# Kernel tuning notes

Measured on AMD Instinct MI355X. Metric: run time of the kernel, lower is better.

Reference implementation:

```python
import jax, jax.numpy as jnp
import numpy as np

B, S, D_MODEL, H = 2, 2048, 1024, 16
D_K = D_MODEL // H
THETA = 10000.0


def setup_inputs() -> dict:
    key = jax.random.key(0)
    k1, k2, k3 = jax.random.split(key, 3)
    x = jax.random.normal(k1, (B, S, D_MODEL), dtype=jnp.float32)
    token_positions = jnp.tile(jnp.arange(S, dtype=jnp.int32), (B, 1))
    qkv_w = jax.random.normal(k2, (3 * D_MODEL, D_MODEL), dtype=jnp.float32) * (D_MODEL ** -0.5)
    out_w = jax.random.normal(k3, (D_MODEL, D_MODEL), dtype=jnp.float32) * (D_MODEL ** -0.5)
    return {"x": x, "token_positions": token_positions, "qkv_w": qkv_w, "out_w": out_w}


def _apply_rope(t, pos):
    # t: [B, H, S, d_k], pos: [B, S]
    half = D_K // 2
    inv_freq = THETA ** (-jnp.arange(0, half, dtype=jnp.float32) * 2.0 / D_K)  # [half]
    ang = pos.astype(jnp.float32)[:, None, :, None] * inv_freq  # [B,1,S,half]
    cos, sin = jnp.cos(ang), jnp.sin(ang)
    t1 = t[..., 0::2]
    t2 = t[..., 1::2]
    r1 = t1 * cos - t2 * sin
    r2 = t1 * sin + t2 * cos
    # interleave back: [..., half, 2] -> [..., d_k]
    return jnp.stack([r1, r2], axis=-1).reshape(t.shape)


def reference(x, token_positions, qkv_w, out_w):
    # fused QKV projection (no bias)
    qkv = jnp.einsum('bsd,ed->bse', x, qkv_w)  # [B,S,3*D_MODEL]
    qkv = qkv.reshape(B, S, 3, H, D_K)
    q = jnp.transpose(qkv[:, :, 0], (0, 2, 1, 3))  # [B,H,S,d_k]
    k = jnp.transpose(qkv[:, :, 1], (0, 2, 1, 3))
    v = jnp.transpose(qkv[:, :, 2], (0, 2, 1, 3))
    q = _apply_rope(q, token_positions)
    k = _apply_rope(k, token_positions)
    scores = jnp.einsum('bhqd,bhkd->bhqk', q, k) / jnp.sqrt(jnp.asarray(D_K, x.dtype))
    causal = jnp.tril(jnp.ones((S, S), dtype=bool))
    neg_inf = jnp.finfo(scores.dtype).min
    scores = jnp.where(causal, scores, neg_inf)
    attn = jax.nn.softmax(scores, axis=-1)
    out = jnp.einsum('bhqk,bhkd->bhqd', attn, v)  # [B,H,S,d_k]
    out = jnp.transpose(out, (0, 2, 1, 3)).reshape(B, S, D_MODEL)
    return jnp.einsum('bsd,ed->bse', out, out_w)
```

## Files before the change

### kernel.cpp

```cpp
#include <hip/hip_runtime.h>
#include <cstdint>

typedef unsigned short u16;
typedef unsigned int u32;
typedef __attribute__((ext_vector_type(8))) short short8;
typedef __attribute__((ext_vector_type(4))) float f32x4;

static constexpr int Bc = 2, Sc = 2048, DMc = 1024, Hc = 16, DKc = 64;
static constexpr int Mc = Bc * Sc;
static constexpr int BHSc = Bc * Hc * Sc;

#if __has_builtin(__builtin_amdgcn_exp2f)
#define EXP2F(x) __builtin_amdgcn_exp2f(x)
#else
#define EXP2F(x) exp2f(x)
#endif

__device__ __forceinline__ float b2f(u16 u) { return __uint_as_float((u32)u << 16); }
__device__ __forceinline__ u16 f2b(float f) {
  u32 x = __float_as_uint(f);
  return (u16)((x + 0x7fffu + ((x >> 16) & 1u)) >> 16);
}
__device__ __forceinline__ u32 pack2(float lo, float hi) {
  return (u32)f2b(lo) | ((u32)f2b(hi) << 16);
}
__device__ __forceinline__ u32 cvtpk(float lo, float hi) {
  u32 r;
  asm("v_cvt_pk_bf16_f32 %0, %1, %2" : "=v"(r) : "v"(lo), "v"(hi));
  return r;
}

__global__ __launch_bounds__(256)
void cvt3_k(const float* __restrict__ x, const float* __restrict__ qw,
            const float* __restrict__ ow,
            u16* __restrict__ xb, u16* __restrict__ qwb, u16* __restrict__ owb)
{
  const int i = blockIdx.x * 256 + threadIdx.x;
  const float* src; u16* dst; int j;
  if (i < 524288)      { src = x;  dst = xb;  j = i; }
  else if (i < 917504) { src = qw; dst = qwb; j = i - 524288; }
  else                 { src = ow; dst = owb; j = i - 917504; }
  const float4 a = *(const float4*)(src + (size_t)j * 8);
  const float4 b = *(const float4*)(src + (size_t)j * 8 + 4);
  uint4 o;
  o.x = cvtpk(a.x, a.y);
  o.y = cvtpk(a.z, a.w);
  o.z = cvtpk(b.x, b.y);
  o.w = cvtpk(b.z, b.w);
  *(uint4*)(dst + (size_t)j * 8) = o;
}

template <typename OutT>
__global__ __launch_bounds__(256, 2)
void gemm_bt128(const u16* __restrict__ A, const u16* __restrict__ W,
                OutT* __restrict__ C, int M, int N, int K)
{
  __shared__ u16 As[128 * 32];
  __shared__ u16 Bs[128 * 32];
  const int t = threadIdx.x;
  const int w = t >> 6, l = t & 63;
  const int wr = w >> 1, wc = w & 1;
  const int l4 = l >> 4, l15 = l & 15;
  const int bm = blockIdx.x, bn = blockIdx.y;

  f32x4 acc[4][4] = {};

  const int rowA = bm * 128, rowB = bn * 128;
  const int sr = l >> 2, sk = (l & 3) * 8;

  for (int k0 = 0; k0 < K; k0 += 32) {
    __syncthreads();
#pragma unroll
    for (int i = 0; i < 2; ++i) {
      const int chunk = i * 4 + w;
      const u16* ga = A + (size_t)(rowA + chunk * 16 + sr) * K + k0 + sk;
      const u16* gb = W + (size_t)(rowB + chunk * 16 + sr) * K + k0 + sk;
      __builtin_amdgcn_global_load_lds((const __attribute__((address_space(1))) void*)ga,
                                       (__attribute__((address_space(3))) void*)(As + chunk * 512), 16, 0, 0);
      __builtin_amdgcn_global_load_lds((const __attribute__((address_space(1))) void*)gb,
                                       (__attribute__((address_space(3))) void*)(Bs + chunk * 512), 16, 0, 0);
    }
    __syncthreads();
    short8 af[4], bf[4];
#pragma unroll
    for (int m = 0; m < 4; ++m)
      af[m] = *(const short8*)(As + (wr * 64 + m * 16 + l15) * 32 + l4 * 8);
#pragma unroll
    for (int n = 0; n < 4; ++n)
      bf[n] = *(const short8*)(Bs + (wc * 64 + n * 16 + l15) * 32 + l4 * 8);
#pragma unroll
    for (int m = 0; m < 4; ++m)
#pragma unroll
      for (int n = 0; n < 4; ++n)
        acc[m][n] = __builtin_amdgcn_mfma_f32_16x16x32_bf16(af[m], bf[n], acc[m][n], 0, 0, 0);
  }

#pragma unroll
  for (int m = 0; m < 4; ++m) {
    const int r0 = rowA + wr * 64 + m * 16 + l4 * 4;
#pragma unroll
    for (int n = 0; n < 4; ++n) {
      const int c0 = rowB + wc * 64 + n * 16 + l15;
#pragma unroll
      for (int r = 0; r < 4; ++r) {
        const float v = acc[m][n][r];
        if constexpr (sizeof(OutT) == 2)
          C[(size_t)(r0 + r) * N + c0] = (OutT)f2b(v);
        else
          C[(size_t)(r0 + r) * N + c0] = (OutT)v;
      }
    }
  }
}

__global__ void rope_table_k(float2* __restrict__ tab)
{
  const int idx = blockIdx.x * 256 + threadIdx.x;
  const int p = idx >> 5, i = idx & 31;
  const float invf = powf(10000.0f, -(float)(2 * i) / 64.0f);
  const float ang = (float)p * invf;
  tab[idx] = make_float2(cosf(ang), sinf(ang));
}

__global__ __launch_bounds__(256)
void rope_reshape_k(const u16* __restrict__ qkv, const int* __restrict__ tokpos,
                    const float2* __restrict__ tab,
                    u16* __restrict__ Q, u16* __restrict__ K, u16* __restrict__ Vt)
{
  __shared__ u16 Vs[64][72];
  const int t = threadIdx.x;
  const int st = blockIdx.x, h = blockIdx.y, b = blockIdx.z;

  {
    const int sl = t >> 2, iq = t & 3;
    const int s = st * 64 + sl;
    const int p = tokpos[b * Sc + s];
    const size_t row = (size_t)(b * Sc + s) * 3 * DMc + h * DKc + iq * 16;
    const size_t orow = ((size_t)(b * Hc + h) * Sc + s) * DKc + iq * 16;
#pragma unroll
    for (int which = 0; which < 2; ++which) {
      const u16* g = qkv + row + which * DMc;
      uint4 va = *(const uint4*)g;
      uint4 vb = *(const uint4*)(g + 8);
      u32 in[8] = {va.x, va.y, va.z, va.w, vb.x, vb.y, vb.z, vb.w};
      const float scale = (which == 0) ? 0.18033688011112f : 1.0f;
      u32 ow[8];
#pragma unroll
      for (int j = 0; j < 8; ++j) {
        const float2 cs = tab[p * 32 + iq * 8 + j];
        const float t1 = b2f((u16)(in[j] & 0xffffu));
        const float t2 = b2f((u16)(in[j] >> 16));
        ow[j] = cvtpk((t1 * cs.x - t2 * cs.y) * scale, (t1 * cs.y + t2 * cs.x) * scale);
      }
      u16* dst = (which == 0 ? Q : K) + orow;
      *(uint4*)dst = make_uint4(ow[0], ow[1], ow[2], ow[3]);
      *(uint4*)(dst + 8) = make_uint4(ow[4], ow[5], ow[6], ow[7]);
    }
  }
#pragma unroll
  for (int it = 0; it < 2; ++it) {
    const int sv = it * 32 + (t >> 3);
    const int d0 = (t & 7) * 8;
    const u16* g = qkv + (size_t)(b * Sc + st * 64 + sv) * 3 * DMc + 2 * DMc + h * DKc + d0;
    *(uint4*)&Vs[sv][d0] = *(const uint4*)g;
  }
  __syncthreads();
  {
    const int d = t >> 2, s0 = (t & 3) * 16;
    u16 tmp[16];
#pragma unroll
    for (int j = 0; j < 16; ++j) tmp[j] = Vs[s0 + j][d];
    u16* dst = Vt + ((size_t)(b * Hc + h) * DKc + d) * Sc + st * 64 + s0;
    *(uint4*)dst = *(const uint4*)tmp;
    *(uint4*)(dst + 8) = *(const uint4*)(tmp + 8);
  }
}

__global__ __launch_bounds__(256, 4)
void attn_k(const u16* __restrict__ Q, const u16* __restrict__ K,
            const u16* __restrict__ Vt, float* __restrict__ Opart,
            float2* __restrict__ ML)
{
  __shared__ u16 Kls[2][64 * 64];
  __shared__ u16 Vls[2][64 * 64];

  const int t = threadIdx.x, w = t >> 6, l = t & 63;
  const int l4 = l >> 4, l15 = l & 15;

  int bid = blockIdx.x;
  bid = (bid & 7) * 128 + (bid >> 3);
  const int p = bid & 15, part = (bid >> 4) & 1, h = (bid >> 5) & 15, b = bid >> 9;

  const int bh = b * Hc + h;
  const u16* Qb = Q + (size_t)bh * Sc * DKc;
  const u16* Kb = K + (size_t)bh * Sc * DKc;
  const u16* Vb = Vt + (size_t)bh * DKc * Sc;
  const int swz = (l15 & 7) << 4;

  const int qt0 = 31 - p, qt1 = p;
  const int q00 = qt0 * 64 + w * 16, q01 = qt1 * 64 + w * 16;
  const int n0 = (qt0 + 2 - part) >> 1, n1 = (qt1 + 2 - part) >> 1;
  const int ntot = n0 + n1;

  const short8 qf0a = *(const short8*)(Qb + (size_t)(q00 + l15) * DKc + l4 * 8);
  const short8 qf0b = *(const short8*)(Qb + (size_t)(q00 + l15) * DKc + 32 + l4 * 8);
  const short8 qf1a = *(const short8*)(Qb + (size_t)(q01 + l15) * DKc + l4 * 8);
  const short8 qf1b = *(const short8*)(Qb + (size_t)(q01 + l15) * DKc + 32 + l4 * 8);

  int srow[2], scol[2];
#pragma unroll
  for (int j = 0; j < 2; ++j) {
    const int e = j * 256 + t;
    srow[j] = e >> 3;
    scol[j] = (((e & 7) * 16) ^ ((srow[j] & 7) << 4)) >> 1;
  }
  auto stage = [&](int buf, int kv0) {
#pragma unroll
    for (int j = 0; j < 2; ++j) {
      const u16* gk = Kb + (size_t)(kv0 + srow[j]) * DKc + scol[j];
      __builtin_amdgcn_global_load_lds((const __attribute__((address_space(1))) void*)gk,
          (__attribute__((address_space(3))) void*)(&Kls[buf][0] + (j * 256 + w * 64) * 8), 16, 0, 0);
    }
#pragma unroll
    for (int j = 0; j < 2; ++j) {
      const u16* gv = Vb + (size_t)srow[j] * Sc + kv0 + scol[j];
      __builtin_amdgcn_global_load_lds((const __attribute__((address_space(1))) void*)gv,
          (__attribute__((address_space(3))) void*)(&Vls[buf][0] + (j * 256 + w * 64) * 8), 16, 0, 0);
    }
  };
  auto kvof = [&](int i) {
    return ((i < n0) ? (part + 2 * i) : (part + 2 * (i - n0))) * 64;
  };

  f32x4 o[4] = {};
  float m = -1e30f, lsum = 0.f;
  int qcur = q00;
  short8 qfA = qf0a, qfB = qf0b;

  auto epi = [&](int qbase) {
    const size_t pbase = ((size_t)part * Bc * Hc + bh) * Sc;
    if (l < 16) ML[pbase + qbase + l15] = make_float2(m, lsum);
#pragma unroll
    for (int dc = 0; dc < 4; ++dc)
#pragma unroll
      for (int r = 0; r < 4; ++r)
        Opart[(pbase + qbase + l4 * 4 + r) * 64 + dc * 16 + l15] = o[dc][r];
  };

  stage(0, kvof(0));
  for (int i = 0; i < ntot; ++i) {
    const int buf = i & 1;
    const int kv0 = kvof(i);
    if (i + 1 < ntot) {
      stage(buf ^ 1, kvof(i + 1));
      asm volatile("s_waitcnt vmcnt(4)" ::: "memory");
    } else {
      asm volatile("s_waitcnt vmcnt(0)" ::: "memory");
    }
    __builtin_amdgcn_s_barrier();

    const char* Kbuf = (const char*)&Kls[buf][0];
    const char* Vbuf = (const char*)&Vls[buf][0];
    char* Pw = (char*)&Kls[buf][0] + w * 2048;

    f32x4 sc[4];
    __builtin_amdgcn_s_setprio(1);
#pragma unroll
    for (int c = 0; c < 4; ++c) {
      const int rb = (c * 16 + l15) * 128;
      const short8 ka  = *(const short8*)(Kbuf + rb + ((l4 * 16) ^ swz));
      const short8 kb2 = *(const short8*)(Kbuf + rb + ((64 + l4 * 16) ^ swz));
      f32x4 z = {0.f, 0.f, 0.f, 0.f};
      z = __builtin_amdgcn_mfma_f32_16x16x32_bf16(ka, qfA, z, 0, 0, 0);
      z = __builtin_amdgcn_mfma_f32_16x16x32_bf16(kb2, qfB, z, 0, 0, 0);
      sc[c] = z;
    }
    __builtin_amdgcn_s_setprio(0);
    if (kv0 + 63 > qcur) {
#pragma unroll
      for (int c = 0; c < 4; ++c) {
        const int kvr = kv0 + c * 16 + l4 * 4;
#pragma unroll
        for (int r = 0; r < 4; ++r)
          if (kvr + r > qcur + l15) sc[c][r] = -1e30f;
      }
    }
    float pmax = -1e30f;
#pragma unroll
    for (int c = 0; c < 4; ++c)
      pmax = fmaxf(pmax, fmaxf(fmaxf(sc[c][0], sc[c][1]), fmaxf(sc[c][2], sc[c][3])));
    pmax = fmaxf(pmax, __shfl_xor(pmax, 16));
    pmax = fmaxf(pmax, __shfl_xor(pmax, 32));
    if (!__all(pmax - m <= 8.0f)) {
      const float mnew = fmaxf(m, pmax);
      const float fac = EXP2F(m - mnew);
      float f4[4];
#pragma unroll
      for (int r = 0; r < 4; ++r) f4[r] = __shfl(fac, l4 * 4 + r);
#pragma unroll
      for (int dc = 0; dc < 4; ++dc) {
        o[dc][0] *= f4[0]; o[dc][1] *= f4[1];
        o[dc][2] *= f4[2]; o[dc][3] *= f4[3];
      }
      lsum *= fac;
      m = mnew;
    }
    float rs = 0.f;
    u32 pk[4][2];
#pragma unroll
    for (int c = 0; c < 4; ++c) {
      const float p0 = EXP2F(sc[c][0] - m);
      const float p1 = EXP2F(sc[c][1] - m);
      const float p2 = EXP2F(sc[c][2] - m);
      const float p3 = EXP2F(sc[c][3] - m);
      rs += (p0 + p1) + (p2 + p3);
      pk[c][0] = cvtpk(p0, p1);
      pk[c][1] = cvtpk(p2, p3);
    }
    rs += __shfl_xor(rs, 16);
    rs += __shfl_xor(rs, 32);
    lsum += rs;

    asm volatile("s_waitcnt lgkmcnt(0)" ::: "memory");
    __builtin_amdgcn_s_barrier();

#pragma unroll
    for (int c = 0; c < 4; ++c) {
      uint2 u; u.x = pk[c][0]; u.y = pk[c][1];
      *(uint2*)(Pw + ((l15 * 128 + c * 32 + l4 * 8) ^ swz)) = u;
    }
    __builtin_amdgcn_s_setprio(1);
#pragma unroll
    for (int kv2 = 0; kv2 < 2; ++kv2) {
      const short8 pa = *(const short8*)(Pw + ((l15 * 128 + kv2 * 64 + l4 * 16) ^ swz));
#pragma unroll
      for (int dc = 0; dc < 4; ++dc) {
        const short8 vf = *(const short8*)(Vbuf + (dc * 16 + l15) * 128 + ((kv2 * 64 + l4 * 16) ^ swz));
        o[dc] = __builtin_amdgcn_mfma_f32_16x16x32_bf16(pa, vf, o[dc], 0, 0, 0);
      }
    }
    __builtin_amdgcn_s_setprio(0);
    asm volatile("s_waitcnt lgkmcnt(0)" ::: "memory");
    __builtin_amdgcn_s_barrier();

    if (i == n0 - 1) {
      epi(q00);
#pragma unroll
      for (int dc = 0; dc < 4; ++dc) o[dc] = f32x4{0.f, 0.f, 0.f, 0.f};
      m = -1e30f; lsum = 0.f;
      qcur = q01; qfA = qf1a; qfB = qf1b;
    }
  }
  epi(q01);
}

__global__ __launch_bounds__(256)
void combine_k(const float* __restrict__ Opart, const float2* __restrict__ ML,
               u16* __restrict__ Oa)
{
  const int idx = blockIdx.x * 256 + threadIdx.x;
  const int row = idx >> 4, c4 = idx & 15;
  const float2 a = ML[row], bm = ML[BHSc + row];
  const float m = fmaxf(a.x, bm.x);
  const float w0 = EXP2F(a.x - m), w1 = EXP2F(bm.x - m);
  const float inv = 1.0f / (w0 * a.y + w1 * bm.y);
  const float4 o0 = *(const float4*)(Opart + (size_t)row * 64 + c4 * 4);
  const float4 o1 = *(const float4*)(Opart + ((size_t)BHSc + row) * 64 + c4 * 4);
  const float r0 = (w0 * o0.x + w1 * o1.x) * inv;
  const float r1 = (w0 * o0.y + w1 * o1.y) * inv;
  const float r2 = (w0 * o0.z + w1 * o1.z) * inv;
  const float r3 = (w0 * o0.w + w1 * o1.w) * inv;
  const int s = row & (Sc - 1), bh = row >> 11, b = bh >> 4, h = bh & 15;
  uint2 pk;
  pk.x = cvtpk(r0, r1);
  pk.y = cvtpk(r2, r3);
  *(uint2*)(Oa + ((size_t)(b * Sc + s) * DMc + h * DKc + c4 * 4)) = pk;
}

extern "C" void kernel_launch(void* const* d_in, const int* in_sizes, int n_in,
                              void* d_out, int out_size, void* d_ws, size_t ws_size,
                              hipStream_t stream)
{
  const float* x      = (const float*)d_in[0];
  const int*   tokpos = (const int*)d_in[1];
  const float* qkv_w  = (const float*)d_in[2];
  const float* out_w  = (const float*)d_in[3];
  float* out = (float*)d_out;

  char* ws = (char*)d_ws;
  size_t off = 0;
  u16*   qkv   = (u16*)(ws + off);
  u16*   xb    = (u16*)(ws + off + 25165824);
  u16*   qwb   = (u16*)(ws + off + 33554432);
  float* Opart = (float*)(ws + off);
  float2* ML   = (float2*)(ws + off + 33554432);
  off += 39845888;
  u16* owb = (u16*)(ws + off); off += (size_t)DMc * DMc * 2;
  u16* Qr  = (u16*)(ws + off); off += (size_t)Bc * Hc * Sc * DKc * 2;
  u16* Kr  = (u16*)(ws + off); off += (size_t)Bc * Hc * Sc * DKc * 2;
  u16* Vt  = (u16*)(ws + off); off += (size_t)Bc * Hc * DKc * Sc * 2;
  u16* Oa  = (u16*)(ws + off); off += (size_t)Mc * DMc * 2;
  float2* tab = (float2*)(ws + off); off += (size_t)Sc * 32 * sizeof(float2);

  cvt3_k<<<4096, 256, 0, stream>>>(x, qkv_w, out_w, xb, qwb, owb);
  rope_table_k<<<(Sc * 32) / 256, 256, 0, stream>>>(tab);
  gemm_bt128<u16><<<dim3(Mc / 128, 3 * DMc / 128), 256, 0, stream>>>(xb, qwb, qkv, Mc, 3 * DMc, DMc);
  rope_reshape_k<<<dim3(Sc / 64, Hc, Bc), 256, 0, stream>>>(qkv, tokpos, tab, Qr, Kr, Vt);
  attn_k<<<1024, 256, 0, stream>>>(Qr, Kr, Vt, Opart, ML);
  combine_k<<<BHSc * 16 / 256, 256, 0, stream>>>(Opart, ML, Oa);
  gemm_bt128<float><<<dim3(Mc / 128, DMc / 128), 256, 0, stream>>>(Oa, owb, out, Mc, DMc, DMc);
}
```

Before: 125.9 us.

## Fuse RoPE and head reshape into QKV GEMM epilogue; store attention partials as bf16

The QKV GEMM epilogue now applies RoPE (using lane shuffles to pair even and odd dims), the Q scale, and the head-major scatter directly. This removes the intermediate qkv buffer and the separate rope/reshape pass. V is still written head-major and transposed by a smaller vtrans kernel. The attention partial outputs are also stored as bf16 instead of fp32, halving combine traffic at some precision cost. The epilogue writes remain scalar 2-byte stores with strided addresses, which may be poorly coalesced.

```diff
diff --git a/kernel.cpp b/kernel.cpp
--- a/kernel.cpp
+++ b/kernel.cpp
@@ -17,13 +17,6 @@
 #endif
 
 __device__ __forceinline__ float b2f(u16 u) { return __uint_as_float((u32)u << 16); }
-__device__ __forceinline__ u16 f2b(float f) {
-  u32 x = __float_as_uint(f);
-  return (u16)((x + 0x7fffu + ((x >> 16) & 1u)) >> 16);
-}
-__device__ __forceinline__ u32 pack2(float lo, float hi) {
-  return (u32)f2b(lo) | ((u32)f2b(hi) << 16);
-}
 __device__ __forceinline__ u32 cvtpk(float lo, float hi) {
   u32 r;
   asm("v_cvt_pk_bf16_f32 %0, %1, %2" : "=v"(r) : "v"(lo), "v"(hi));
@@ -50,10 +43,13 @@
   *(uint4*)(dst + (size_t)j * 8) = o;
 }
 
-template <typename OutT>
+template <int EPI>
 __global__ __launch_bounds__(256, 2)
 void gemm_bt128(const u16* __restrict__ A, const u16* __restrict__ W,
-                OutT* __restrict__ C, int M, int N, int K)
+                float* __restrict__ Cf,
+                const int* __restrict__ tokpos, const float2* __restrict__ tab,
+                u16* __restrict__ Qo, u16* __restrict__ Ko, u16* __restrict__ Vo,
+                int M, int N, int K)
 {
   __shared__ u16 As[128 * 32];
   __shared__ u16 Bs[128 * 32];
@@ -95,19 +91,52 @@
         acc[m][n] = __builtin_amdgcn_mfma_f32_16x16x32_bf16(af[m], bf[n], acc[m][n], 0, 0, 0);
   }
 
-#pragma unroll
-  for (int m = 0; m < 4; ++m) {
-    const int r0 = rowA + wr * 64 + m * 16 + l4 * 4;
-#pragma unroll
-    for (int n = 0; n < 4; ++n) {
-      const int c0 = rowB + wc * 64 + n * 16 + l15;
-#pragma unroll
-      for (int r = 0; r < 4; ++r) {
-        const float v = acc[m][n][r];
-        if constexpr (sizeof(OutT) == 2)
-          C[(size_t)(r0 + r) * N + c0] = (OutT)f2b(v);
-        else
-          C[(size_t)(r0 + r) * N + c0] = (OutT)v;
+  if constexpr (EPI == 2) {
+    const int whichW = bn >> 3;
+    const int hh = (bn & 7) * 2 + wc;
+    u16* dst = (whichW == 0) ? Qo : (whichW == 1 ? Ko : Vo);
+    int pos[4][4];
+    if (whichW < 2) {
+#pragma unroll
+      for (int m = 0; m < 4; ++m)
+#pragma unroll
+        for (int r = 0; r < 4; ++r)
+          pos[m][r] = tokpos[rowA + wr * 64 + m * 16 + l4 * 4 + r];
+    }
+#pragma unroll
+    for (int m = 0; m < 4; ++m) {
+#pragma unroll
+      for (int n = 0; n < 4; ++n) {
+        const int d = n * 16 + l15;
+#pragma unroll
+        for (int r = 0; r < 4; ++r) {
+          const int sg = rowA + wr * 64 + m * 16 + l4 * 4 + r;
+          const int bb = sg >> 11, ss = sg & 2047;
+          const size_t addr = ((size_t)(bb * Hc + hh) * Sc + ss) * DKc + d;
+          const float v = acc[m][n][r];
+          if (whichW == 2) {
+            dst[addr] = (u16)cvtpk(v, v);
+          } else {
+            const float vp = __shfl_xor(v, 1);
+            const float2 cs = tab[pos[m][r] * 32 + (d >> 1)];
+            float res = (l15 & 1) ? (vp * cs.y + v * cs.x)
+                                  : (v * cs.x - vp * cs.y);
+            if (whichW == 0) res *= 0.18033688011112f;
+            dst[addr] = (u16)cvtpk(res, res);
+          }
+        }
+      }
+    }
+  } else {
+#pragma unroll
+    for (int m = 0; m < 4; ++m) {
+      const int r0 = rowA + wr * 64 + m * 16 + l4 * 4;
+#pragma unroll
+      for (int n = 0; n < 4; ++n) {
+        const int c0 = rowB + wc * 64 + n * 16 + l15;
+#pragma unroll
+        for (int r = 0; r < 4; ++r)
+          Cf[(size_t)(r0 + r) * N + c0] = acc[m][n][r];
       }
     }
   }
@@ -123,62 +152,31 @@
 }
 
 __global__ __launch_bounds__(256)
-void rope_reshape_k(const u16* __restrict__ qkv, const int* __restrict__ tokpos,
-                    const float2* __restrict__ tab,
-                    u16* __restrict__ Q, u16* __restrict__ K, u16* __restrict__ Vt)
-{
-  __shared__ u16 Vs[64][72];
+void vtrans_k(const u16* __restrict__ Vc, u16* __restrict__ Vt)
+{
+  __shared__ u16 T[64][72];
   const int t = threadIdx.x;
   const int st = blockIdx.x, h = blockIdx.y, b = blockIdx.z;
-
-  {
-    const int sl = t >> 2, iq = t & 3;
-    const int s = st * 64 + sl;
-    const int p = tokpos[b * Sc + s];
-    const size_t row = (size_t)(b * Sc + s) * 3 * DMc + h * DKc + iq * 16;
-    const size_t orow = ((size_t)(b * Hc + h) * Sc + s) * DKc + iq * 16;
-#pragma unroll
-    for (int which = 0; which < 2; ++which) {
-      const u16* g = qkv + row + which * DMc;
-      uint4 va = *(const uint4*)g;
-      uint4 vb = *(const uint4*)(g + 8);
-      u32 in[8] = {va.x, va.y, va.z, va.w, vb.x, vb.y, vb.z, vb.w};
-      const float scale = (which == 0) ? 0.18033688011112f : 1.0f;
-      u32 ow[8];
-#pragma unroll
-      for (int j = 0; j < 8; ++j) {
-        const float2 cs = tab[p * 32 + iq * 8 + j];
-        const float t1 = b2f((u16)(in[j] & 0xffffu));
-        const float t2 = b2f((u16)(in[j] >> 16));
-        ow[j] = cvtpk((t1 * cs.x - t2 * cs.y) * scale, (t1 * cs.y + t2 * cs.x) * scale);
-      }
-      u16* dst = (which == 0 ? Q : K) + orow;
-      *(uint4*)dst = make_uint4(ow[0], ow[1], ow[2], ow[3]);
-      *(uint4*)(dst + 8) = make_uint4(ow[4], ow[5], ow[6], ow[7]);
-    }
-  }
+  const size_t bh = (size_t)b * Hc + h;
 #pragma unroll
   for (int it = 0; it < 2; ++it) {
     const int sv = it * 32 + (t >> 3);
     const int d0 = (t & 7) * 8;
-    const u16* g = qkv + (size_t)(b * Sc + st * 64 + sv) * 3 * DMc + 2 * DMc + h * DKc + d0;
-    *(uint4*)&Vs[sv][d0] = *(const uint4*)g;
+    *(uint4*)&T[sv][d0] = *(const uint4*)(Vc + (bh * Sc + st * 64 + sv) * DKc + d0);
   }
   __syncthreads();
-  {
-    const int d = t >> 2, s0 = (t & 3) * 16;
-    u16 tmp[16];
-#pragma unroll
-    for (int j = 0; j < 16; ++j) tmp[j] = Vs[s0 + j][d];
-    u16* dst = Vt + ((size_t)(b * Hc + h) * DKc + d) * Sc + st * 64 + s0;
-    *(uint4*)dst = *(const uint4*)tmp;
-    *(uint4*)(dst + 8) = *(const uint4*)(tmp + 8);
-  }
+  const int d = t >> 2, s0 = (t & 3) * 16;
+  u16 tmp[16];
+#pragma unroll
+  for (int j = 0; j < 16; ++j) tmp[j] = T[s0 + j][d];
+  u16* dst = Vt + (bh * DKc + d) * Sc + st * 64 + s0;
+  *(uint4*)dst = *(const uint4*)tmp;
+  *(uint4*)(dst + 8) = *(const uint4*)(tmp + 8);
 }
 
 __global__ __launch_bounds__(256, 4)
 void attn_k(const u16* __restrict__ Q, const u16* __restrict__ K,
-            const u16* __restrict__ Vt, float* __restrict__ Opart,
+            const u16* __restrict__ Vt, u16* __restrict__ Opart,
             float2* __restrict__ ML)
 {
   __shared__ u16 Kls[2][64 * 64];
@@ -244,7 +242,8 @@
     for (int dc = 0; dc < 4; ++dc)
 #pragma unroll
       for (int r = 0; r < 4; ++r)
-        Opart[(pbase + qbase + l4 * 4 + r) * 64 + dc * 16 + l15] = o[dc][r];
+        Opart[(pbase + qbase + l4 * 4 + r) * 64 + dc * 16 + l15] =
+            (u16)cvtpk(o[dc][r], o[dc][r]);
   };
 
   stage(0, kvof(0));
@@ -355,21 +354,21 @@
 }
 
 __global__ __launch_bounds__(256)
-void combine_k(const float* __restrict__ Opart, const float2* __restrict__ ML,
+void combine_k(const u16* __restrict__ Opart, const float2* __restrict__ ML,
                u16* __restrict__ Oa)
 {
   const int idx = blockIdx.x * 256 + threadIdx.x;
   const int row = idx >> 4, c4 = idx & 15;
-  const float2 a = ML[row], bm = ML[BHSc + row];
-  const float m = fmaxf(a.x, bm.x);
-  const float w0 = EXP2F(a.x - m), w1 = EXP2F(bm.x - m);
-  const float inv = 1.0f / (w0 * a.y + w1 * bm.y);
-  const float4 o0 = *(const float4*)(Opart + (size_t)row * 64 + c4 * 4);
-  const float4 o1 = *(const float4*)(Opart + ((size_t)BHSc + row) * 64 + c4 * 4);
-  const float r0 = (w0 * o0.x + w1 * o1.x) * inv;
-  const float r1 = (w0 * o0.y + w1 * o1.y) * inv;
-  const float r2 = (w0 * o0.z + w1 * o1.z) * inv;
-  const float r3 = (w0 * o0.w + w1 * o1.w) * inv;
+  const float2 a = ML[row], bm2 = ML[BHSc + row];
+  const float m = fmaxf(a.x, bm2.x);
+  const float w0 = EXP2F(a.x - m), w1 = EXP2F(bm2.x - m);
+  const float inv = 1.0f / (w0 * a.y + w1 * bm2.y);
+  const uint2 u0 = *(const uint2*)(Opart + (size_t)row * 64 + c4 * 4);
+  const uint2 u1 = *(const uint2*)(Opart + ((size_t)BHSc + row) * 64 + c4 * 4);
+  const float r0 = (w0 * b2f((u16)u0.x) + w1 * b2f((u16)u1.x)) * inv;
+  const float r1 = (w0 * b2f((u16)(u0.x >> 16)) + w1 * b2f((u16)(u1.x >> 16))) * inv;
+  const float r2 = (w0 * b2f((u16)u0.y) + w1 * b2f((u16)u1.y)) * inv;
+  const float r3 = (w0 * b2f((u16)(u0.y >> 16)) + w1 * b2f((u16)(u1.y >> 16))) * inv;
   const int s = row & (Sc - 1), bh = row >> 11, b = bh >> 4, h = bh & 15;
   uint2 pk;
   pk.x = cvtpk(r0, r1);
@@ -389,24 +388,25 @@
 
   char* ws = (char*)d_ws;
   size_t off = 0;
-  u16*   qkv   = (u16*)(ws + off);
-  u16*   xb    = (u16*)(ws + off + 25165824);
-  u16*   qwb   = (u16*)(ws + off + 33554432);
-  float* Opart = (float*)(ws + off);
-  float2* ML   = (float2*)(ws + off + 33554432);
-  off += 39845888;
-  u16* owb = (u16*)(ws + off); off += (size_t)DMc * DMc * 2;
-  u16* Qr  = (u16*)(ws + off); off += (size_t)Bc * Hc * Sc * DKc * 2;
-  u16* Kr  = (u16*)(ws + off); off += (size_t)Bc * Hc * Sc * DKc * 2;
-  u16* Vt  = (u16*)(ws + off); off += (size_t)Bc * Hc * DKc * Sc * 2;
-  u16* Oa  = (u16*)(ws + off); off += (size_t)Mc * DMc * 2;
+  u16* xb    = (u16*)(ws + off); off += (size_t)Mc * DMc * 2;
+  u16* qwb   = (u16*)(ws + off); off += (size_t)3 * DMc * DMc * 2;
+  u16* owb   = (u16*)(ws + off); off += (size_t)DMc * DMc * 2;
+  u16* Qr    = (u16*)(ws + off); off += (size_t)BHSc * DKc * 2;
+  u16* Kr    = (u16*)(ws + off); off += (size_t)BHSc * DKc * 2;
+  u16* Vc    = (u16*)(ws + off); off += (size_t)BHSc * DKc * 2;
+  u16* Vt    = (u16*)(ws + off); off += (size_t)BHSc * DKc * 2;
+  u16* Opart = (u16*)(ws + off); off += (size_t)2 * BHSc * DKc * 2;
+  float2* ML = (float2*)(ws + off); off += (size_t)2 * BHSc * sizeof(float2);
+  u16* Oa    = (u16*)(ws + off); off += (size_t)Mc * DMc * 2;
   float2* tab = (float2*)(ws + off); off += (size_t)Sc * 32 * sizeof(float2);
 
   cvt3_k<<<4096, 256, 0, stream>>>(x, qkv_w, out_w, xb, qwb, owb);
   rope_table_k<<<(Sc * 32) / 256, 256, 0, stream>>>(tab);
-  gemm_bt128<u16><<<dim3(Mc / 128, 3 * DMc / 128), 256, 0, stream>>>(xb, qwb, qkv, Mc, 3 * DMc, DMc);
-  rope_reshape_k<<<dim3(Sc / 64, Hc, Bc), 256, 0, stream>>>(qkv, tokpos, tab, Qr, Kr, Vt);
+  gemm_bt128<2><<<dim3(Mc / 128, 3 * DMc / 128), 256, 0, stream>>>(
+      xb, qwb, nullptr, tokpos, tab, Qr, Kr, Vc, Mc, 3 * DMc, DMc);
+  vtrans_k<<<dim3(Sc / 64, Hc, Bc), 256, 0, stream>>>(Vc, Vt);
   attn_k<<<1024, 256, 0, stream>>>(Qr, Kr, Vt, Opart, ML);
   combine_k<<<BHSc * 16 / 256, 256, 0, stream>>>(Opart, ML, Oa);
-  gemm_bt128<float><<<dim3(Mc / 128, DMc / 128), 256, 0, stream>>>(Oa, owb, out, Mc, DMc, DMc);
-}
+  gemm_bt128<0><<<dim3(Mc / 128, DMc / 128), 256, 0, stream>>>(
+      Oa, owb, out, nullptr, nullptr, nullptr, nullptr, nullptr, Mc, DMc, DMc);
+}
```

Result: no change. 127.4 us (+1.1%).

## Store attention partials in bf16 and move K/V prefetch after the loop barrier

Applied to the files above, without the earlier changes.

The split-KV attention kernel now writes its partial output tiles as bf16 instead of fp32, and the combine kernel reads and widens them. This halves the partial-output write and read traffic, at the cost of extra rounding before the softmax merge. The double-buffer loop is also rescheduled: it waits for all outstanding loads, barriers, then issues the next tile's stage. This removes the trailing lgkmcnt wait and second barrier per iteration, trading one barrier for less overlap slack on the prefetch.

```diff
diff --git a/kernel.cpp b/kernel.cpp
--- a/kernel.cpp
+++ b/kernel.cpp
@@ -20,9 +20,6 @@
 __device__ __forceinline__ u16 f2b(float f) {
   u32 x = __float_as_uint(f);
   return (u16)((x + 0x7fffu + ((x >> 16) & 1u)) >> 16);
-}
-__device__ __forceinline__ u32 pack2(float lo, float hi) {
-  return (u32)f2b(lo) | ((u32)f2b(hi) << 16);
 }
 __device__ __forceinline__ u32 cvtpk(float lo, float hi) {
   u32 r;
@@ -178,7 +175,7 @@
 
 __global__ __launch_bounds__(256, 4)
 void attn_k(const u16* __restrict__ Q, const u16* __restrict__ K,
-            const u16* __restrict__ Vt, float* __restrict__ Opart,
+            const u16* __restrict__ Vt, u16* __restrict__ Opart,
             float2* __restrict__ ML)
 {
   __shared__ u16 Kls[2][64 * 64];
@@ -244,20 +241,17 @@
     for (int dc = 0; dc < 4; ++dc)
 #pragma unroll
       for (int r = 0; r < 4; ++r)
-        Opart[(pbase + qbase + l4 * 4 + r) * 64 + dc * 16 + l15] = o[dc][r];
+        Opart[(pbase + qbase + l4 * 4 + r) * 64 + dc * 16 + l15] =
+            (u16)cvtpk(o[dc][r], o[dc][r]);
   };
 
   stage(0, kvof(0));
   for (int i = 0; i < ntot; ++i) {
     const int buf = i & 1;
     const int kv0 = kvof(i);
-    if (i + 1 < ntot) {
-      stage(buf ^ 1, kvof(i + 1));
-      asm volatile("s_waitcnt vmcnt(4)" ::: "memory");
-    } else {
-      asm volatile("s_waitcnt vmcnt(0)" ::: "memory");
-    }
+    asm volatile("s_waitcnt vmcnt(0)" ::: "memory");
     __builtin_amdgcn_s_barrier();
+    if (i + 1 < ntot) stage(buf ^ 1, kvof(i + 1));
 
     const char* Kbuf = (const char*)&Kls[buf][0];
     const char* Vbuf = (const char*)&Vls[buf][0];
@@ -340,8 +334,6 @@
       }
     }
     __builtin_amdgcn_s_setprio(0);
-    asm volatile("s_waitcnt lgkmcnt(0)" ::: "memory");
-    __builtin_amdgcn_s_barrier();
 
     if (i == n0 - 1) {
       epi(q00);
@@ -355,21 +347,21 @@
 }
 
 __global__ __launch_bounds__(256)
-void combine_k(const float* __restrict__ Opart, const float2* __restrict__ ML,
+void combine_k(const u16* __restrict__ Opart, const float2* __restrict__ ML,
                u16* __restrict__ Oa)
 {
   const int idx = blockIdx.x * 256 + threadIdx.x;
   const int row = idx >> 4, c4 = idx & 15;
-  const float2 a = ML[row], bm = ML[BHSc + row];
-  const float m = fmaxf(a.x, bm.x);
-  const float w0 = EXP2F(a.x - m), w1 = EXP2F(bm.x - m);
-  const float inv = 1.0f / (w0 * a.y + w1 * bm.y);
-  const float4 o0 = *(const float4*)(Opart + (size_t)row * 64 + c4 * 4);
-  const float4 o1 = *(const float4*)(Opart + ((size_t)BHSc + row) * 64 + c4 * 4);
-  const float r0 = (w0 * o0.x + w1 * o1.x) * inv;
-  const float r1 = (w0 * o0.y + w1 * o1.y) * inv;
-  const float r2 = (w0 * o0.z + w1 * o1.z) * inv;
-  const float r3 = (w0 * o0.w + w1 * o1.w) * inv;
+  const float2 a = ML[row], bm2 = ML[BHSc + row];
+  const float m = fmaxf(a.x, bm2.x);
+  const float w0 = EXP2F(a.x - m), w1 = EXP2F(bm2.x - m);
+  const float inv = 1.0f / (w0 * a.y + w1 * bm2.y);
+  const uint2 u0 = *(const uint2*)(Opart + (size_t)row * 64 + c4 * 4);
+  const uint2 u1 = *(const uint2*)(Opart + ((size_t)BHSc + row) * 64 + c4 * 4);
+  const float r0 = (w0 * b2f((u16)u0.x) + w1 * b2f((u16)u1.x)) * inv;
+  const float r1 = (w0 * b2f((u16)(u0.x >> 16)) + w1 * b2f((u16)(u1.x >> 16))) * inv;
+  const float r2 = (w0 * b2f((u16)u0.y) + w1 * b2f((u16)u1.y)) * inv;
+  const float r3 = (w0 * b2f((u16)(u0.y >> 16)) + w1 * b2f((u16)(u1.y >> 16))) * inv;
   const int s = row & (Sc - 1), bh = row >> 11, b = bh >> 4, h = bh & 15;
   uint2 pk;
   pk.x = cvtpk(r0, r1);
@@ -392,13 +384,13 @@
   u16*   qkv   = (u16*)(ws + off);
   u16*   xb    = (u16*)(ws + off + 25165824);
   u16*   qwb   = (u16*)(ws + off + 33554432);
-  float* Opart = (float*)(ws + off);
+  u16*   Opart = (u16*)(ws + off);
   float2* ML   = (float2*)(ws + off + 33554432);
   off += 39845888;
   u16* owb = (u16*)(ws + off); off += (size_t)DMc * DMc * 2;
-  u16* Qr  = (u16*)(ws + off); off += (size_t)Bc * Hc * Sc * DKc * 2;
-  u16* Kr  = (u16*)(ws + off); off += (size_t)Bc * Hc * Sc * DKc * 2;
-  u16* Vt  = (u16*)(ws + off); off += (size_t)Bc * Hc * DKc * Sc * 2;
+  u16* Qr  = (u16*)(ws + off); off += (size_t)BHSc * DKc * 2;
+  u16* Kr  = (u16*)(ws + off); off += (size_t)BHSc * DKc * 2;
+  u16* Vt  = (u16*)(ws + off); off += (size_t)BHSc * DKc * 2;
   u16* Oa  = (u16*)(ws + off); off += (size_t)Mc * DMc * 2;
   float2* tab = (float2*)(ws + off); off += (size_t)Sc * 32 * sizeof(float2);
 
```

New measurement: 123.5 us. About the same (-1.9%).
